# Performance work log

Hardware: AMD Instinct MI355X
Metric: run time of the kernel (lower is better)

## Reference

```python
import jax, jax.numpy as jnp
import numpy as np
from jax import lax

B, A, C, M = 8, 100000, 80, 32
ALPHA, GAMMA = 0.25, 2.0


def _calc_iou(a, b):
    # a: [A,4] anchors, b: [M,4] gt boxes -> [A,M]
    area = (b[:, 2] - b[:, 0]) * (b[:, 3] - b[:, 1])
    iw = jnp.clip(jnp.minimum(a[:, None, 2], b[None, :, 2]) - jnp.maximum(a[:, None, 0], b[None, :, 0]), 0.0)
    ih = jnp.clip(jnp.minimum(a[:, None, 3], b[None, :, 3]) - jnp.maximum(a[:, None, 1], b[None, :, 1]), 0.0)
    inter = iw * ih
    ua = jnp.clip(((a[:, 2] - a[:, 0]) * (a[:, 3] - a[:, 1]))[:, None] + area[None, :] - inter, 1e-8)
    return inter / ua


def _per_image(cls_p, reg, ann, anchor):
    # cls_p: [A,C], reg: [A,4], ann: [M,9], anchor: [A,4]
    p = jnp.clip(cls_p, 1e-4, 1.0 - 1e-4)
    iou = _calc_iou(anchor, ann[:, :4])            # [A,M]
    iou_max = jnp.max(iou, axis=1)                 # [A]
    iou_arg = jnp.argmax(iou, axis=1)              # [A]
    assigned = ann[iou_arg]                        # [A,9]
    pos = iou_max >= 0.5
    num_pos = jnp.sum(pos)

    # targets: -1 = ignore, 0 = background, one-hot for positives
    t = jnp.where(iou_max[:, None] < 0.4, 0.0, -1.0)
    cls_idx = lax.stop_gradient(assigned[:, 4]).astype(jnp.int32)
    t = jnp.where(pos[:, None], jax.nn.one_hot(cls_idx, C, dtype=p.dtype), t)

    alpha_f = jnp.where(t == 1.0, ALPHA, 1.0 - ALPHA)
    fw = jnp.where(t == 1.0, 1.0 - p, p)
    bce = -(t * jnp.log(p) + (1.0 - t) * jnp.log(1.0 - p))
    cls_loss = jnp.where(t != -1.0, alpha_f * fw ** GAMMA * bce, 0.0)
    cls_l = jnp.sum(cls_loss) / jnp.maximum(num_pos.astype(p.dtype), 1.0)

    aw = anchor[:, 2] - anchor[:, 0]
    ah = anchor[:, 3] - anchor[:, 1]
    acx = anchor[:, 0] + 0.5 * aw
    acy = anchor[:, 1] + 0.5 * ah
    gw_raw = assigned[:, 2] - assigned[:, 0]
    gh_raw = assigned[:, 3] - assigned[:, 1]
    gcx = assigned[:, 0] + 0.5 * gw_raw
    gcy = assigned[:, 1] + 0.5 * gh_raw
    gw = jnp.clip(gw_raw, 1.0)
    gh = jnp.clip(gh_raw, 1.0)
    tgt = jnp.stack([(gcx - acx) / aw, (gcy - acy) / ah,
                     jnp.log(gw / aw), jnp.log(gh / ah)], axis=1)
    tgt = tgt / jnp.array([0.1, 0.1, 0.2, 0.2], dtype=p.dtype)
    diff = jnp.abs(tgt - reg)
    sl1 = jnp.where(diff <= 1.0 / 9.0, 0.5 * 9.0 * diff ** 2, diff - 0.5 / 9.0)
    denom = jnp.maximum(num_pos.astype(p.dtype) * 4.0, 1.0)
    reg_l = jnp.where(num_pos > 0,
                      jnp.sum(jnp.where(pos[:, None], sl1, 0.0)) / denom,
                      jnp.zeros((), p.dtype))
    return cls_l, reg_l


def setup_inputs() -> dict:
    key = jax.random.key(0)
    k = jax.random.split(key, 8)
    classifications = jax.random.uniform(k[0], (B, A, C), jnp.float32, 1e-3, 1.0 - 1e-3)
    regressions = 0.1 * jax.random.normal(k[1], (B, A, 4), jnp.float32)
    ax0 = jax.random.uniform(k[2], (A,), jnp.float32, 0.0, 900.0)
    ay0 = jax.random.uniform(k[3], (A,), jnp.float32, 0.0, 900.0)
    awh = jax.random.uniform(k[4], (A, 2), jnp.float32, 16.0, 128.0)
    anchors = jnp.stack([ax0, ay0, ax0 + awh[:, 0], ay0 + awh[:, 1]], axis=1)[None]
    b0 = jax.random.uniform(k[5], (B, M, 2), jnp.float32, 0.0, 800.0)
    bwh = jax.random.uniform(k[6], (B, M, 2), jnp.float32, 8.0, 200.0)
    labels = jax.random.randint(k[7], (B, M, 1), 0, C).astype(jnp.float32)
    extra = jnp.zeros((B, M, 4), jnp.float32)  # cols 5..8: instance id + geo filler
    annotations = jnp.concatenate([b0, b0 + bwh, labels, extra], axis=-1)  # [B,M,9]
    return dict(classifications=classifications, regressions=regressions,
                anchors=anchors, annotations=annotations)


def reference(classifications, regressions, anchors, annotations):
    anchor = anchors[0]
    cls_l, reg_l = jax.vmap(_per_image, in_axes=(0, 0, 0, None))(
        classifications, regressions, annotations, anchor)
    return jnp.stack([jnp.mean(cls_l), jnp.mean(reg_l)])
```

## Files before the change

### kernel.cpp

```cpp
#include <hip/hip_runtime.h>

#define A_N 100000
#define B_N 8
#define C_N 80
#define M_N 32


__global__ __launch_bounds__(256) void focal_main(
    const float4* __restrict__ cls4,
    const float4* __restrict__ reg4,
    const float4* __restrict__ anc4,
    const float*  __restrict__ ann,
    float* __restrict__ cls_sum, float* __restrict__ reg_sum, int* __restrict__ npos)
{
    __shared__ float annL[M_N][6];
    __shared__ unsigned char stateL[256];
    __shared__ unsigned char clsIdxL[256];
    __shared__ float redA[4];
    __shared__ int   redI[4];
    __shared__ float redB[4];

    const int b   = blockIdx.y;
    const int a0  = blockIdx.x * 256;
    const int tid = threadIdx.x;

    for (int i = tid; i < M_N * 5; i += 256) {
        int m = i / 5, c = i % 5;
        annL[m][c] = ann[(b * M_N + m) * 9 + c];
    }
    __syncthreads();
    if (tid < M_N) {
        annL[tid][5] = (annL[tid][2] - annL[tid][0]) * (annL[tid][3] - annL[tid][1]);
    }
    __syncthreads();

    const int a = a0 + tid;
    const bool valid = a < A_N;
    float regacc = 0.0f;
    bool pos = false;
    int st = 1;
    int ci = 0;

    if (valid) {
        float4 an = anc4[a];
        float aw = an.z - an.x, ah = an.w - an.y;
        float aArea = aw * ah;
        float best = -1.0f; int bidx = 0;
        #pragma unroll 8
        for (int m = 0; m < M_N; ++m) {
            float iw = fminf(an.z, annL[m][2]) - fmaxf(an.x, annL[m][0]);
            float ih = fminf(an.w, annL[m][3]) - fmaxf(an.y, annL[m][1]);
            iw = fmaxf(iw, 0.0f); ih = fmaxf(ih, 0.0f);
            float inter = iw * ih;
            float ua = fmaxf(aArea + annL[m][5] - inter, 1e-8f);
            float iou = inter / ua;
            if (iou > best) { best = iou; bidx = m; }
        }
        pos = best >= 0.5f;
        st  = pos ? 2 : (best < 0.4f ? 0 : 1);
        ci  = (int)annL[bidx][4];

        if (pos) {
            float4 r = reg4[(size_t)b * A_N + a];
            float gx0 = annL[bidx][0], gy0 = annL[bidx][1];
            float gx1 = annL[bidx][2], gy1 = annL[bidx][3];
            float gwr = gx1 - gx0, ghr = gy1 - gy0;
            float gcx = gx0 + 0.5f * gwr, gcy = gy0 + 0.5f * ghr;
            float gw = fmaxf(gwr, 1.0f), gh = fmaxf(ghr, 1.0f);
            float acx = an.x + 0.5f * aw, acy = an.y + 0.5f * ah;
            float t0 = (gcx - acx) / aw * 10.0f;
            float t1 = (gcy - acy) / ah * 10.0f;
            float t2 = __logf(gw / aw) * 5.0f;
            float t3 = __logf(gh / ah) * 5.0f;
            float d0 = fabsf(t0 - r.x), d1 = fabsf(t1 - r.y);
            float d2 = fabsf(t2 - r.z), d3 = fabsf(t3 - r.w);
            const float th = 1.0f / 9.0f;
            const float hs = 0.5f / 9.0f;
            regacc  = (d0 <= th) ? 4.5f * d0 * d0 : d0 - hs;
            regacc += (d1 <= th) ? 4.5f * d1 * d1 : d1 - hs;
            regacc += (d2 <= th) ? 4.5f * d2 * d2 : d2 - hs;
            regacc += (d3 <= th) ? 4.5f * d3 * d3 : d3 - hs;
        }
    }
    stateL[tid]  = (unsigned char)st;
    clsIdxL[tid] = (unsigned char)ci;

    unsigned long long bal = __ballot(pos);
    #pragma unroll
    for (int o = 32; o > 0; o >>= 1) regacc += __shfl_down(regacc, o, 64);
    int lane = tid & 63, wid = tid >> 6;
    if (lane == 0) { redA[wid] = regacc; redI[wid] = __popcll(bal); }
    __syncthreads();
    if (tid == 0) {
        float rs = redA[0] + redA[1] + redA[2] + redA[3];
        int   np = redI[0] + redI[1] + redI[2] + redI[3];
        if (rs != 0.0f) atomicAdd(&reg_sum[b], rs);
        if (np)         atomicAdd(&npos[b], np);
    }

    const float4* cbase = cls4 + ((size_t)b * A_N + a0) * 20;
    const int nA = min(256, A_N - a0);
    const int n4 = nA * 20;
    float clsacc = 0.0f;
    for (int i = tid; i < n4; i += 256) {
        int la  = i / 20;
        int st2 = stateL[la];
        if (st2 == 1) continue;
        float4 v = cbase[i];
        int ciL = clsIdxL[la];
        int c0  = (i % 20) * 4;
        float pv[4] = {v.x, v.y, v.z, v.w};
        #pragma unroll
        for (int j = 0; j < 4; ++j) {
            float p = fminf(fmaxf(pv[j], 1e-4f), 1.0f - 1e-4f);
            bool one = (st2 == 2) && (c0 + j == ciL);
            float alphaf = one ? 0.25f : 0.75f;
            float w      = one ? 1.0f - p : p;
            float arg    = one ? p : 1.0f - p;
            clsacc += alphaf * w * w * (-__logf(arg));
        }
    }
    #pragma unroll
    for (int o = 32; o > 0; o >>= 1) clsacc += __shfl_down(clsacc, o, 64);
    if (lane == 0) redB[wid] = clsacc;
    __syncthreads();
    if (tid == 0) {
        float cs = redB[0] + redB[1] + redB[2] + redB[3];
        atomicAdd(&cls_sum[b], cs);
    }
}

__global__ void focal_finalize(const float* __restrict__ cls_sum,
                               const float* __restrict__ reg_sum,
                               const int* __restrict__ npos,
                               float* __restrict__ out)
{
    if (threadIdx.x == 0) {
        float c = 0.0f, r = 0.0f;
        for (int b = 0; b < B_N; ++b) {
            float np = (float)npos[b];
            c += cls_sum[b] / fmaxf(np, 1.0f);
            r += (npos[b] > 0) ? reg_sum[b] / (4.0f * np) : 0.0f;
        }
        out[0] = c / (float)B_N;
        out[1] = r / (float)B_N;
    }
}

extern "C" void kernel_launch(void* const* d_in, const int* in_sizes, int n_in,
                              void* d_out, int out_size, void* d_ws, size_t ws_size,
                              hipStream_t stream) {
    const float* cls = (const float*)d_in[0];
    const float* reg = (const float*)d_in[1];
    const float* anc = (const float*)d_in[2];
    const float* ann = (const float*)d_in[3];

    float* ws      = (float*)d_ws;
    float* cls_sum = ws;
    float* reg_sum = ws + 8;
    int*   npos    = (int*)(ws + 16);

    hipMemsetAsync(d_ws, 0, 24 * sizeof(float), stream);

    dim3 grid((A_N + 255) / 256, B_N);
    focal_main<<<grid, 256, 0, stream>>>(
        (const float4*)cls, (const float4*)reg, (const float4*)anc, ann,
        cls_sum, reg_sum, npos);

    focal_finalize<<<1, 64, 0, stream>>>(cls_sum, reg_sum, npos, (float*)d_out);
}
```

Before: 386.7 us.

## Split anchor assignment from classification streaming into separate kernels

Moves IoU assignment and regression loss into a first kernel that writes a packed per-anchor state/class array. A second kernel streams the classification tensor in large contiguous chunks with nontemporal vector loads, an unrolled loop and dual accumulators, then looks up the per-anchor metadata. This decouples the compute-heavy assignment from the bandwidth-bound streaming pass. The cost is an extra launch, a small metadata round trip through global memory, and loading ignored anchors that were previously skipped.

Measured after the change: 387.3 us. About the same (+0.1%).

```diff
diff --git a/kernel.cpp b/kernel.cpp
--- a/kernel.cpp
+++ b/kernel.cpp
@@ -4,21 +4,23 @@
 #define B_N 8
 #define C_N 80
 #define M_N 32
-
-
-__global__ __launch_bounds__(256) void focal_main(
-    const float4* __restrict__ cls4,
+#define IMG4 2000000
+#define CHUNK4 8192
+#define BX ((IMG4 + CHUNK4 - 1) / CHUNK4)
+
+typedef float vfloat4 __attribute__((ext_vector_type(4)));
+
+
+__global__ __launch_bounds__(256) void focal_assign(
     const float4* __restrict__ reg4,
     const float4* __restrict__ anc4,
     const float*  __restrict__ ann,
-    float* __restrict__ cls_sum, float* __restrict__ reg_sum, int* __restrict__ npos)
+    unsigned short* __restrict__ meta,
+    float* __restrict__ reg_sum, int* __restrict__ npos)
 {
     __shared__ float annL[M_N][6];
-    __shared__ unsigned char stateL[256];
-    __shared__ unsigned char clsIdxL[256];
     __shared__ float redA[4];
     __shared__ int   redI[4];
-    __shared__ float redB[4];
 
     const int b   = blockIdx.y;
     const int a0  = blockIdx.x * 256;
@@ -35,13 +37,10 @@
     __syncthreads();
 
     const int a = a0 + tid;
-    const bool valid = a < A_N;
     float regacc = 0.0f;
     bool pos = false;
-    int st = 1;
-    int ci = 0;
-
-    if (valid) {
+
+    if (a < A_N) {
         float4 an = anc4[a];
         float aw = an.z - an.x, ah = an.w - an.y;
         float aArea = aw * ah;
@@ -57,8 +56,9 @@
             if (iou > best) { best = iou; bidx = m; }
         }
         pos = best >= 0.5f;
-        st  = pos ? 2 : (best < 0.4f ? 0 : 1);
-        ci  = (int)annL[bidx][4];
+        int st = pos ? 2 : (best < 0.4f ? 0 : 1);
+        int ci = (int)annL[bidx][4];
+        meta[(size_t)b * A_N + a] = (unsigned short)(st | (ci << 2));
 
         if (pos) {
             float4 r = reg4[(size_t)b * A_N + a];
@@ -82,8 +82,6 @@
             regacc += (d3 <= th) ? 4.5f * d3 * d3 : d3 - hs;
         }
     }
-    stateL[tid]  = (unsigned char)st;
-    clsIdxL[tid] = (unsigned char)ci;
 
     unsigned long long bal = __ballot(pos);
     #pragma unroll
@@ -97,37 +95,72 @@
         if (rs != 0.0f) atomicAdd(&reg_sum[b], rs);
         if (np)         atomicAdd(&npos[b], np);
     }
-
-    const float4* cbase = cls4 + ((size_t)b * A_N + a0) * 20;
-    const int nA = min(256, A_N - a0);
-    const int n4 = nA * 20;
-    float clsacc = 0.0f;
-    for (int i = tid; i < n4; i += 256) {
-        int la  = i / 20;
-        int st2 = stateL[la];
-        if (st2 == 1) continue;
-        float4 v = cbase[i];
-        int ciL = clsIdxL[la];
-        int c0  = (i % 20) * 4;
-        float pv[4] = {v.x, v.y, v.z, v.w};
-        #pragma unroll
-        for (int j = 0; j < 4; ++j) {
-            float p = fminf(fmaxf(pv[j], 1e-4f), 1.0f - 1e-4f);
-            bool one = (st2 == 2) && (c0 + j == ciL);
-            float alphaf = one ? 0.25f : 0.75f;
-            float w      = one ? 1.0f - p : p;
-            float arg    = one ? p : 1.0f - p;
-            clsacc += alphaf * w * w * (-__logf(arg));
-        }
-    }
+}
+
+__device__ __forceinline__ float focal_term(vfloat4 v, int st2, int ciL, int c0)
+{
+    float notIgn = (st2 != 1) ? 1.0f : 0.0f;
+    bool  isPos  = (st2 == 2);
+    float pv[4] = {v.x, v.y, v.z, v.w};
+    float term = 0.0f;
+    #pragma unroll
+    for (int j = 0; j < 4; ++j) {
+        float p = fminf(fmaxf(pv[j], 1e-4f), 1.0f - 1e-4f);
+        bool one = isPos && (c0 + j == ciL);
+        float alphaf = one ? 0.25f : 0.75f;
+        float w      = one ? 1.0f - p : p;
+        float arg    = one ? p : 1.0f - p;
+        term += alphaf * w * w * (-__logf(arg));
+    }
+    return notIgn * term;
+}
+
+__global__ __launch_bounds__(256) void focal_cls(
+    const vfloat4* __restrict__ cls4,
+    const unsigned short* __restrict__ meta,
+    float* __restrict__ cls_sum)
+{
+    __shared__ float redB[4];
+    const int b   = blockIdx.y;
+    const int bx  = blockIdx.x;
+    const int tid = threadIdx.x;
+    const int i0  = bx * CHUNK4;
+    const vfloat4* __restrict__ cbase = cls4 + (size_t)b * IMG4 + i0;
+    const unsigned short* __restrict__ mbase = meta + (size_t)b * A_N;
+
+    float acc0 = 0.0f, acc1 = 0.0f;
+
+    if (i0 + CHUNK4 <= IMG4) {
+        #pragma unroll 4
+        for (int k = 0; k < CHUNK4 / 256; ++k) {
+            int io = (k << 8) + tid;
+            vfloat4 v = __builtin_nontemporal_load(cbase + io);
+            int i  = i0 + io;
+            int la = i / 20;
+            int c0 = (i - la * 20) * 4;
+            unsigned short m = mbase[la];
+            float t = focal_term(v, m & 3, m >> 2, c0);
+            if (k & 1) acc1 += t; else acc0 += t;
+        }
+    } else {
+        const int n = IMG4 - i0;
+        for (int io = tid; io < n; io += 256) {
+            vfloat4 v = __builtin_nontemporal_load(cbase + io);
+            int i  = i0 + io;
+            int la = i / 20;
+            int c0 = (i - la * 20) * 4;
+            unsigned short m = mbase[la];
+            acc0 += focal_term(v, m & 3, m >> 2, c0);
+        }
+    }
+
+    float clsacc = acc0 + acc1;
     #pragma unroll
     for (int o = 32; o > 0; o >>= 1) clsacc += __shfl_down(clsacc, o, 64);
+    int lane = tid & 63, wid = tid >> 6;
     if (lane == 0) redB[wid] = clsacc;
     __syncthreads();
-    if (tid == 0) {
-        float cs = redB[0] + redB[1] + redB[2] + redB[3];
-        atomicAdd(&cls_sum[b], cs);
-    }
+    if (tid == 0) atomicAdd(&cls_sum[b], redB[0] + redB[1] + redB[2] + redB[3]);
 }
 
 __global__ void focal_finalize(const float* __restrict__ cls_sum,
@@ -159,13 +192,16 @@
     float* cls_sum = ws;
     float* reg_sum = ws + 8;
     int*   npos    = (int*)(ws + 16);
-
-    hipMemsetAsync(d_ws, 0, 24 * sizeof(float), stream);
-
-    dim3 grid((A_N + 255) / 256, B_N);
-    focal_main<<<grid, 256, 0, stream>>>(
-        (const float4*)cls, (const float4*)reg, (const float4*)anc, ann,
-        cls_sum, reg_sum, npos);
+    unsigned short* meta = (unsigned short*)((char*)d_ws + 256);
+
+    (void)hipMemsetAsync(d_ws, 0, 24 * sizeof(float), stream);
+
+    dim3 gridA((A_N + 255) / 256, B_N);
+    focal_assign<<<gridA, 256, 0, stream>>>(
+        (const float4*)reg, (const float4*)anc, ann, meta, reg_sum, npos);
+
+    dim3 gridC(BX, B_N);
+    focal_cls<<<gridC, 256, 0, stream>>>((const vfloat4*)cls, meta, cls_sum);
 
     focal_finalize<<<1, 64, 0, stream>>>(cls_sum, reg_sum, npos, (float*)d_out);
 }
```
